# Kernel tuning notes

Hardware: AMD Instinct MI355X
Metric: run time of the kernel (lower is better)

Reference implementation:

```python
import jax, jax.numpy as jnp
import numpy as np

V, D, H, KVH, HD, I, L, T_MAX, THETA = 32000, 1024, 16, 4, 64, 2816, 2, 2048, 10000.0
EPS = 1e-5


def rmsnorm(x, w):
    return x * jax.lax.rsqrt(jnp.mean(x * x, axis=-1, keepdims=True) + EPS) * w


def rope_cos_sin(T):
    inv = 1.0 / (THETA ** (jnp.arange(0, HD, 2, dtype=jnp.float32) / HD))  # [HD/2]
    ang = jnp.arange(T, dtype=jnp.float32)[:, None] * inv[None, :]         # [T, HD/2]
    return jnp.cos(ang), jnp.sin(ang)


def apply_rope(x, cos, sin):
    # x: [B, T, h, HD]; interleaved complex pairs as in torch.view_as_complex
    x0 = x[..., 0::2]
    x1 = x[..., 1::2]
    c = cos[None, :, None, :]
    s = sin[None, :, None, :]
    o0 = x0 * c - x1 * s
    o1 = x0 * s + x1 * c
    return jnp.stack([o0, o1], axis=-1).reshape(x.shape)


def setup_inputs() -> dict:
    key = jax.random.key(0)
    ks = jax.random.split(key, 12)
    sc = 0.02
    return {
        "toks": jax.random.randint(ks[0], (1, 2048), 0, V),
        "embed": jax.random.normal(ks[1], (V, D), jnp.float32) * sc,
        "Wq": jax.random.normal(ks[2], (L, D, H * HD), jnp.float32) * sc,
        "Wk": jax.random.normal(ks[3], (L, D, KVH * HD), jnp.float32) * sc,
        "Wv": jax.random.normal(ks[4], (L, D, KVH * HD), jnp.float32) * sc,
        "Wo": jax.random.normal(ks[5], (L, H * HD, D), jnp.float32) * sc,
        "Wgate": jax.random.normal(ks[6], (L, D, I), jnp.float32) * sc,
        "Wup": jax.random.normal(ks[7], (L, D, I), jnp.float32) * sc,
        "Wdown": jax.random.normal(ks[8], (L, I, D), jnp.float32) * sc,
        "ln1_w": jnp.ones((L, D), jnp.float32),
        "ln2_w": jnp.ones((L, D), jnp.float32),
        "norm_w": jnp.ones((D,), jnp.float32),
        "Wlm": jax.random.normal(ks[9], (D, V), jnp.float32) * sc,
    }


def reference(toks, embed, Wq, Wk, Wv, Wo, Wgate, Wup, Wdown, ln1_w, ln2_w, norm_w, Wlm):
    B, T = toks.shape
    cos, sin = rope_cos_sin(T)
    causal = jnp.tril(jnp.ones((T, T), dtype=bool))
    add_mask = jnp.where(causal, 0.0, -jnp.inf).astype(jnp.float32)  # [T, T]
    n_rep = H // KVH
    scale = 1.0 / np.sqrt(HD)

    x = embed[toks]  # [B, T, D]
    for l in range(L):
        h = rmsnorm(x, ln1_w[l])
        q = (h @ Wq[l]).reshape(B, T, H, HD)
        k = (h @ Wk[l]).reshape(B, T, KVH, HD)
        v = (h @ Wv[l]).reshape(B, T, KVH, HD)
        q = apply_rope(q, cos, sin)
        k = apply_rope(k, cos, sin)
        k = jnp.repeat(k, n_rep, axis=2)  # GQA repeat_kv -> [B, T, H, HD]
        v = jnp.repeat(v, n_rep, axis=2)
        # materialized scores [B, H, T, T] (faithful to source)
        scores = jnp.einsum('bqhd,bkhd->bhqk', q, k) * scale + add_mask[None, None]
        probs = jax.nn.softmax(scores, axis=-1)
        attn = jnp.einsum('bhqk,bkhd->bqhd', probs, v).reshape(B, T, H * HD)
        x = x + attn @ Wo[l]
        h = rmsnorm(x, ln2_w[l])
        x = x + (jax.nn.silu(h @ Wgate[l]) * (h @ Wup[l])) @ Wdown[l]

    x = rmsnorm(x, norm_w)
    return x @ Wlm  # [B, T, V]
```

## Files before the change

kernel.cpp:

```cpp
#include <hip/hip_runtime.h>

#define T_SEQ 2048
#define DMODEL 1024
#define NH 16
#define NKV 4
#define HEAD_DIM 64
#define FFDIM 2816
#define NVOCAB 32000

#define QBLK 64
#define KBLK 128
#define KSS 72
#define VTS 136
#define PSS 136

using u16 = unsigned short;
typedef __bf16 bf16x8 __attribute__((ext_vector_type(8)));
typedef float f32x4 __attribute__((ext_vector_type(4)));

__device__ __forceinline__ float b2f(u16 u) {
    union { unsigned int i; float f; } v; v.i = ((unsigned int)u) << 16; return v.f;
}
__device__ __forceinline__ u16 f2b(float f) {
    unsigned int u = __builtin_bit_cast(unsigned int, f);
    unsigned int r = (u + 0x7FFFu + ((u >> 16) & 1u)) >> 16;
    return (u16)r;
}
__device__ __forceinline__ void gload16(const u16* g, u16* l) {
    __builtin_amdgcn_global_load_lds(
        (const __attribute__((address_space(1))) void*)g,
        (__attribute__((address_space(3))) void*)l, 16, 0, 0);
}

__global__ __launch_bounds__(256) void embed_kernel(const int* __restrict__ toks,
                                                    const float* __restrict__ emb,
                                                    float* __restrict__ x) {
    int idx = blockIdx.x * 256 + threadIdx.x;
    int t = idx >> 10, d = idx & 1023;
    x[idx] = emb[(size_t)toks[t] * DMODEL + d];
}

__global__ __launch_bounds__(256) void rmsnorm_kernel(const float* __restrict__ x,
                                                      const float* __restrict__ w,
                                                      u16* __restrict__ out) {
    __shared__ float red[256];
    const int row = blockIdx.x, tid = threadIdx.x;
    const float* xr = x + (size_t)row * DMODEL;
    float vals[4]; float ss = 0.f;
#pragma unroll
    for (int i = 0; i < 4; i++) { float v = xr[tid + 256 * i]; vals[i] = v; ss += v * v; }
    red[tid] = ss; __syncthreads();
    for (int s = 128; s > 0; s >>= 1) { if (tid < s) red[tid] += red[tid + s]; __syncthreads(); }
    float inv = rsqrtf(red[0] * (1.0f / DMODEL) + 1e-5f);
#pragma unroll
    for (int i = 0; i < 4; i++) {
        int c = tid + 256 * i;
        out[(size_t)row * DMODEL + c] = f2b(vals[i] * inv * w[c]);
    }
}

__global__ __launch_bounds__(256) void tcast_kernel(const float* __restrict__ in,
                                                    u16* __restrict__ out, int K, int N) {
    __shared__ float tile[32][33];
    int bx = blockIdx.x * 32;
    int by = blockIdx.y * 32;
    int tx = threadIdx.x & 31, ty = threadIdx.x >> 5;
#pragma unroll
    for (int i = 0; i < 32; i += 8)
        tile[ty + i][tx] = in[(size_t)(by + ty + i) * N + bx + tx];
    __syncthreads();
#pragma unroll
    for (int i = 0; i < 32; i += 8)
        out[(size_t)(bx + ty + i) * K + by + tx] = f2b(tile[tx][ty + i]);
}

__global__ __launch_bounds__(256) void vtcast_kernel(const float* __restrict__ fqkv,
                                                     u16* __restrict__ vt) {
    __shared__ float tile[32][33];
    int bx = blockIdx.x * 32;
    int by = blockIdx.y * 32;
    int tx = threadIdx.x & 31, ty = threadIdx.x >> 5;
#pragma unroll
    for (int i = 0; i < 32; i += 8)
        tile[ty + i][tx] = fqkv[(size_t)(by + ty + i) * 1536 + 1280 + bx + tx];
    __syncthreads();
#pragma unroll
    for (int i = 0; i < 32; i += 8)
        vt[(size_t)(bx + ty + i) * T_SEQ + by + tx] = f2b(tile[tx][ty + i]);
}

__global__ __launch_bounds__(256) void gemm_bt_kernel(const u16* __restrict__ A,
                                                      const u16* __restrict__ BT,
                                                      float* __restrict__ C,
                                                      int N, int K) {
    __shared__ __align__(16) u16 As[2][128 * 32];
    __shared__ __align__(16) u16 Bs[2][128 * 32];
    const int tid = threadIdx.x;
    const int gx = gridDim.x;
    const int nwg = gx * gridDim.y;
    const int hwid = blockIdx.y * gx + blockIdx.x;
    const int q = nwg >> 3, r = nwg & 7;
    const int xcd = hwid & 7, rem = hwid >> 3;
    const int wgid = (xcd < r ? xcd * (q + 1) : r * (q + 1) + (xcd - r) * q) + rem;
    const int brow = wgid % gx, bcol = wgid / gx;

    const int w = tid >> 6, lane = tid & 63;
    const int wr = w >> 1, wc = w & 1;
    const int lg = lane >> 4, lr = lane & 15;

    f32x4 acc[4][4] = {};

    const int srow = w * 32 + (lane >> 2);
    const int scol = (lane & 3) << 3;
    const u16* gA = A + (size_t)(brow * 128 + srow) * K + scol;
    const u16* gB = BT + (size_t)(bcol * 128 + srow) * K + scol;
    const int lofs0 = (w * 32) * 32;
    const int lofs1 = (w * 32 + 16) * 32;

    const int nt = K >> 5;
    gload16(gA, &As[0][lofs0]);
    gload16(gA + (size_t)16 * K, &As[0][lofs1]);
    gload16(gB, &Bs[0][lofs0]);
    gload16(gB + (size_t)16 * K, &Bs[0][lofs1]);
    __syncthreads();

    int cur = 0;
    for (int t = 0; t < nt; t++) {
        if (t + 1 < nt) {
            const int kb = (t + 1) << 5;
            gload16(gA + kb, &As[cur ^ 1][lofs0]);
            gload16(gA + (size_t)16 * K + kb, &As[cur ^ 1][lofs1]);
            gload16(gB + kb, &Bs[cur ^ 1][lofs0]);
            gload16(gB + (size_t)16 * K + kb, &Bs[cur ^ 1][lofs1]);
        }
        bf16x8 aF[4], bF[4];
#pragma unroll
        for (int m = 0; m < 4; m++)
            aF[m] = *(const bf16x8*)(&As[cur][(wr * 64 + m * 16 + lr) * 32 + lg * 8]);
#pragma unroll
        for (int n = 0; n < 4; n++)
            bF[n] = *(const bf16x8*)(&Bs[cur][(wc * 64 + n * 16 + lr) * 32 + lg * 8]);
#pragma unroll
        for (int m = 0; m < 4; m++)
#pragma unroll
            for (int n = 0; n < 4; n++)
                acc[m][n] = __builtin_amdgcn_mfma_f32_16x16x32_bf16(aF[m], bF[n], acc[m][n], 0, 0, 0);
        __syncthreads();
        cur ^= 1;
    }

#pragma unroll
    for (int m = 0; m < 4; m++)
#pragma unroll
        for (int n = 0; n < 4; n++)
#pragma unroll
            for (int j = 0; j < 4; j++) {
                int row = brow * 128 + wr * 64 + m * 16 + lg * 4 + j;
                int col = bcol * 128 + wc * 64 + n * 16 + lr;
                C[(size_t)row * N + col] = acc[m][n][j];
            }
}

__device__ __forceinline__ int bs_off(int c, int k) {
    return c * 40 + ((((k >> 3) ^ ((c >> 3) & 3)) << 3) | (k & 7));
}

__global__ __launch_bounds__(256) void gemm_f32b_kernel(const u16* __restrict__ A,
                                                        const float* __restrict__ B,
                                                        float* __restrict__ C,
                                                        int N, int K) {
    __shared__ __align__(16) u16 As[128 * 40];
    __shared__ __align__(16) u16 Bs[128 * 40];
    const int tid = threadIdx.x;
    const int brow = blockIdx.y, bcol = blockIdx.x;
    const int wid = tid >> 6, lane = tid & 63;
    const int wr = wid >> 1, wc = wid & 1;
    const int lg = lane >> 4, lr = lane & 15;

    f32x4 acc[4][4] = {};
    const int ar = tid >> 2, ac = (tid & 3) << 3;
    const int bk = tid >> 4, bc = (tid & 15) << 3;

    for (int kb = 0; kb < K; kb += 32) {
        {
            const u16* ga = A + (size_t)(brow * 128 + ar) * K + kb + ac;
            *(uint4*)(&As[ar * 40 + ac]) = *(const uint4*)ga;
            *(uint4*)(&As[(ar + 64) * 40 + ac]) = *(const uint4*)(ga + (size_t)64 * K);
        }
        {
            const float* gb = B + (size_t)(kb + bk) * N + bcol * 128 + bc;
            float4 a0 = *(const float4*)gb;
            float4 a1 = *(const float4*)(gb + 4);
            float4 b0 = *(const float4*)(gb + (size_t)16 * N);
            float4 b1 = *(const float4*)(gb + (size_t)16 * N + 4);
            float f0[8] = {a0.x, a0.y, a0.z, a0.w, a1.x, a1.y, a1.z, a1.w};
            float f1[8] = {b0.x, b0.y, b0.z, b0.w, b1.x, b1.y, b1.z, b1.w};
#pragma unroll
            for (int i = 0; i < 8; i++) {
                Bs[bs_off(bc + i, bk)] = f2b(f0[i]);
                Bs[bs_off(bc + i, bk + 16)] = f2b(f1[i]);
            }
        }
        __syncthreads();

        bf16x8 aF[4], bF[4];
#pragma unroll
        for (int m = 0; m < 4; m++)
            aF[m] = *(const bf16x8*)(&As[(wr * 64 + m * 16 + lr) * 40 + lg * 8]);
#pragma unroll
        for (int n = 0; n < 4; n++) {
            int c = wc * 64 + n * 16 + lr;
            bF[n] = *(const bf16x8*)(&Bs[c * 40 + ((lg ^ ((c >> 3) & 3)) << 3)]);
        }
#pragma unroll
        for (int m = 0; m < 4; m++)
#pragma unroll
            for (int n = 0; n < 4; n++)
                acc[m][n] = __builtin_amdgcn_mfma_f32_16x16x32_bf16(aF[m], bF[n], acc[m][n], 0, 0, 0);
        __syncthreads();
    }

#pragma unroll
    for (int m = 0; m < 4; m++)
#pragma unroll
        for (int n = 0; n < 4; n++)
#pragma unroll
            for (int j = 0; j < 4; j++) {
                int row = brow * 128 + wr * 64 + m * 16 + lg * 4 + j;
                int col = bcol * 128 + wc * 64 + n * 16 + lr;
                C[(size_t)row * N + col] = acc[m][n][j];
            }
}

__global__ __launch_bounds__(256) void rope_kernel(const float* __restrict__ in,
                                                   u16* __restrict__ out, int heads,
                                                   int instride, int incoloff) {
    int idx = blockIdx.x * 256 + threadIdx.x;
    int total = T_SEQ * heads * 32;
    if (idx >= total) return;
    int i = idx & 31;
    int rest = idx >> 5;
    int t = rest / heads, hh = rest - t * heads;
    float inv = expf(-(float)i * (9.210340371976184f / 32.0f));
    float ang = (float)t * inv;
    float c = cosf(ang), s = sinf(ang);
    size_t src = (size_t)t * instride + incoloff + hh * HEAD_DIM + 2 * i;
    size_t dst = (size_t)rest * HEAD_DIM + 2 * i;
    float x0 = in[src], x1 = in[src + 1];
    out[dst]     = f2b(x0 * c - x1 * s);
    out[dst + 1] = f2b(x0 * s + x1 * c);
}

__global__ __launch_bounds__(256) void fattn_kernel(const u16* __restrict__ q,
                                                    const u16* __restrict__ k,
                                                    const u16* __restrict__ vt,
                                                    u16* __restrict__ out) {
    __shared__ __align__(16) u16 Ks[KBLK * KSS];
    __shared__ __align__(16) u16 Vt[HEAD_DIM * VTS];
    __shared__ __align__(16) u16 Ps[QBLK * PSS];
    const int tid = threadIdx.x;
    const int qb0 = blockIdx.x * QBLK, h = blockIdx.y, kvh = h >> 2;
    const int w = tid >> 6, lane = tid & 63;
    const int lg = lane >> 4, lr = lane & 15;

    bf16x8 qf0, qf1;
    {
        const u16* src = q + ((size_t)(qb0 + w * 16 + lr) * NH + h) * HEAD_DIM;
        qf0 = *(const bf16x8*)(src + lg * 8);
        qf1 = *(const bf16x8*)(src + 32 + lg * 8);
    }

    f32x4 acc_o[4] = {};
    float m_run[4] = {-1e30f, -1e30f, -1e30f, -1e30f};
    float l_run[4] = {0.f, 0.f, 0.f, 0.f};

    const int ntiles = (qb0 + QBLK - 1) / KBLK + 1;

    for (int kt = 0; kt < ntiles; kt++) {
        const int kb = kt * KBLK;
        __syncthreads();
        for (int c = tid; c < KBLK * 8; c += 256) {
            int row = c >> 3, c8 = (c & 7) << 3;
            *(uint4*)(&Ks[row * KSS + c8]) =
                *(const uint4*)(k + ((size_t)(kb + row) * NKV + kvh) * HEAD_DIM + c8);
        }
        for (int c = tid; c < HEAD_DIM * 16; c += 256) {
            int d = c >> 4, c16 = (c & 15) << 3;
            *(uint4*)(&Vt[d * VTS + c16]) =
                *(const uint4*)(vt + (size_t)(kvh * HEAD_DIM + d) * T_SEQ + kb + c16);
        }
        __syncthreads();

        f32x4 s[8] = {};
#pragma unroll
        for (int n = 0; n < 8; n++) {
            bf16x8 kf0 = *(const bf16x8*)(&Ks[(n * 16 + lr) * KSS + lg * 8]);
            bf16x8 kf1 = *(const bf16x8*)(&Ks[(n * 16 + lr) * KSS + 32 + lg * 8]);
            s[n] = __builtin_amdgcn_mfma_f32_16x16x32_bf16(qf0, kf0, s[n], 0, 0, 0);
            s[n] = __builtin_amdgcn_mfma_f32_16x16x32_bf16(qf1, kf1, s[n], 0, 0, 0);
        }

#pragma unroll
        for (int j = 0; j < 4; j++) {
            int q_g = qb0 + w * 16 + lg * 4 + j;
            float sv[8];
            float tmax = -1e30f;
#pragma unroll
            for (int n = 0; n < 8; n++) {
                float xx = s[n][j] * 0.125f;
                if (kb + n * 16 + lr > q_g) xx = -1e30f;
                sv[n] = xx;
                tmax = fmaxf(tmax, xx);
            }
#pragma unroll
            for (int mm = 1; mm < 16; mm <<= 1) tmax = fmaxf(tmax, __shfl_xor(tmax, mm));
            float mn = fmaxf(m_run[j], tmax);
            float sc = __expf(m_run[j] - mn);
            m_run[j] = mn;
            float rsum = 0.f;
#pragma unroll
            for (int n = 0; n < 8; n++) {
                float p = __expf(sv[n] - mn);
                rsum += p;
                Ps[(w * 16 + lg * 4 + j) * PSS + n * 16 + lr] = f2b(p);
            }
#pragma unroll
            for (int mm = 1; mm < 16; mm <<= 1) rsum += __shfl_xor(rsum, mm);
            l_run[j] = l_run[j] * sc + rsum;
#pragma unroll
            for (int n = 0; n < 4; n++) acc_o[n][j] *= sc;
        }

#pragma unroll
        for (int ks = 0; ks < 4; ks++) {
            bf16x8 pf = *(const bf16x8*)(&Ps[(w * 16 + lr) * PSS + ks * 32 + lg * 8]);
#pragma unroll
            for (int n = 0; n < 4; n++) {
                bf16x8 vf = *(const bf16x8*)(&Vt[(n * 16 + lr) * VTS + ks * 32 + lg * 8]);
                acc_o[n] = __builtin_amdgcn_mfma_f32_16x16x32_bf16(pf, vf, acc_o[n], 0, 0, 0);
            }
        }
    }

#pragma unroll
    for (int n = 0; n < 4; n++)
#pragma unroll
        for (int j = 0; j < 4; j++) {
            int t = qb0 + w * 16 + lg * 4 + j;
            int d = n * 16 + lr;
            out[((size_t)t * NH + h) * HEAD_DIM + d] = f2b(acc_o[n][j] / l_run[j]);
        }
}

__global__ __launch_bounds__(256) void silu_mul_kernel(const float* __restrict__ gu,
                                                       u16* __restrict__ out) {
    int t = blockIdx.x;
    int c = blockIdx.y * 256 + threadIdx.x;
    float gv = gu[(size_t)t * 5632 + c];
    float uv = gu[(size_t)t * 5632 + 2816 + c];
    float s = gv / (1.f + __expf(-gv));
    out[(size_t)t * FFDIM + c] = f2b(s * uv);
}

__global__ __launch_bounds__(256) void add_kernel(float* __restrict__ x,
                                                  const float* __restrict__ y, int n) {
    int i = blockIdx.x * 256 + threadIdx.x;
    if (i < n) x[i] += y[i];
}

extern "C" void kernel_launch(void* const* d_in, const int* in_sizes, int n_in,
                              void* d_out, int out_size, void* d_ws, size_t ws_size,
                              hipStream_t stream) {
    const int*   toks = (const int*)d_in[0];
    const float* emb  = (const float*)d_in[1];
    const float* Wq   = (const float*)d_in[2];
    const float* Wk   = (const float*)d_in[3];
    const float* Wv   = (const float*)d_in[4];
    const float* Wo   = (const float*)d_in[5];
    const float* Wg   = (const float*)d_in[6];
    const float* Wu   = (const float*)d_in[7];
    const float* Wd   = (const float*)d_in[8];
    const float* ln1  = (const float*)d_in[9];
    const float* ln2  = (const float*)d_in[10];
    const float* nw   = (const float*)d_in[11];
    const float* Wlm  = (const float*)d_in[12];

    char* ob = (char*)d_out;
    const size_t MB = 1024 * 1024;
    float* x    = (float*)(ob + 0 * MB);
    float* fqkv = (float*)(ob + 8 * MB);
    float* fGU  = (float*)(ob + 20 * MB);
    float* fA   = (float*)(ob + 64 * MB);
    u16* vt     = (u16*)  (ob + 72 * MB);
    u16* qb     = (u16*)  (ob + 74 * MB);
    u16* kb     = (u16*)  (ob + 78 * MB);
    u16* attnb  = (u16*)  (ob + 80 * MB);
    u16* ffb    = (u16*)  (ob + 84 * MB);
    size_t woff = 96 * MB;
    auto walloc = [&](size_t elems) {
        u16* p = (u16*)(ob + woff);
        woff += ((elems * 2 + 255) & ~(size_t)255);
        return p;
    };
    u16 *WqkvT[2], *WoT[2], *WguT[2], *WdT[2];
    for (int l = 0; l < 2; l++) {
        WqkvT[l] = walloc((size_t)1536 * DMODEL);
        WoT[l]   = walloc((size_t)DMODEL * DMODEL);
        WguT[l]  = walloc((size_t)5632 * DMODEL);
        WdT[l]   = walloc((size_t)DMODEL * FFDIM);
    }
    u16* h = (u16*)d_ws;
    bool ws_big = ws_size >= 72 * MB;
    u16* WlmT = ws_big ? (u16*)((char*)d_ws + 4 * MB) : nullptr;
    (void)in_sizes; (void)n_in; (void)out_size;

    dim3 blk(256);
    auto tcast = [&](const float* in, u16* out, int K, int N) {
        tcast_kernel<<<dim3(N / 32, K / 32), blk, 0, stream>>>(in, out, K, N);
    };
    auto gemm_bt = [&](const u16* A, const u16* BT, float* C, int N, int K) {
        dim3 g(T_SEQ / 128, N / 128);
        gemm_bt_kernel<<<g, blk, 0, stream>>>(A, BT, C, N, K);
    };

    for (int l = 0; l < 2; l++) {
        tcast(Wq + (size_t)l * DMODEL * NH * HEAD_DIM,  WqkvT[l],                    DMODEL, NH * HEAD_DIM);
        tcast(Wk + (size_t)l * DMODEL * NKV * HEAD_DIM, WqkvT[l] + (size_t)1024 * DMODEL, DMODEL, NKV * HEAD_DIM);
        tcast(Wv + (size_t)l * DMODEL * NKV * HEAD_DIM, WqkvT[l] + (size_t)1280 * DMODEL, DMODEL, NKV * HEAD_DIM);
        tcast(Wo + (size_t)l * DMODEL * DMODEL,         WoT[l],  DMODEL, DMODEL);
        tcast(Wg + (size_t)l * DMODEL * FFDIM,          WguT[l],                     DMODEL, FFDIM);
        tcast(Wu + (size_t)l * DMODEL * FFDIM,          WguT[l] + (size_t)FFDIM * DMODEL, DMODEL, FFDIM);
        tcast(Wd + (size_t)l * FFDIM * DMODEL,          WdT[l],  FFDIM, DMODEL);
    }
    if (WlmT) tcast(Wlm, WlmT, DMODEL, NVOCAB);

    embed_kernel<<<dim3(T_SEQ * DMODEL / 256), blk, 0, stream>>>(toks, emb, x);

    for (int l = 0; l < 2; l++) {
        rmsnorm_kernel<<<dim3(T_SEQ), blk, 0, stream>>>(x, ln1 + (size_t)l * DMODEL, h);
        gemm_bt(h, WqkvT[l], fqkv, 1536, DMODEL);
        rope_kernel<<<dim3(T_SEQ * NH * 32 / 256), blk, 0, stream>>>(fqkv, qb, NH, 1536, 0);
        rope_kernel<<<dim3(T_SEQ * NKV * 32 / 256), blk, 0, stream>>>(fqkv, kb, NKV, 1536, 1024);
        vtcast_kernel<<<dim3(8, T_SEQ / 32), blk, 0, stream>>>(fqkv, vt);
        fattn_kernel<<<dim3(T_SEQ / QBLK, NH), blk, 0, stream>>>(qb, kb, vt, attnb);
        gemm_bt(attnb, WoT[l], fA, DMODEL, DMODEL);
        add_kernel<<<dim3(T_SEQ * DMODEL / 256), blk, 0, stream>>>(x, fA, T_SEQ * DMODEL);

        rmsnorm_kernel<<<dim3(T_SEQ), blk, 0, stream>>>(x, ln2 + (size_t)l * DMODEL, h);
        gemm_bt(h, WguT[l], fGU, 5632, DMODEL);
        silu_mul_kernel<<<dim3(T_SEQ, FFDIM / 256), blk, 0, stream>>>(fGU, ffb);
        gemm_bt(ffb, WdT[l], fA, DMODEL, FFDIM);
        add_kernel<<<dim3(T_SEQ * DMODEL / 256), blk, 0, stream>>>(x, fA, T_SEQ * DMODEL);
    }

    rmsnorm_kernel<<<dim3(T_SEQ), blk, 0, stream>>>(x, nw, h);
    if (WlmT) {
        gemm_bt(h, WlmT, (float*)d_out, NVOCAB, DMODEL);
    } else {
        dim3 g(NVOCAB / 128, T_SEQ / 128);
        gemm_f32b_kernel<<<g, blk, 0, stream>>>(h, Wlm, (float*)d_out, NVOCAB, DMODEL);
    }
}
```

Before: 851.1 us.

## Triple-buffer GEMM loads, emit bf16 intermediates, fuse residual add into GEMM epilogue

The GEMM kernel goes from a double-buffered to a triple-buffered LDS pipeline, with explicit vmcnt waits and raw barriers, so global loads for tile t+2 overlap compute on tile t. The QKV and gate/up projections now write bf16 instead of fp32, which halves the traffic into rope, vtcast and silu_mul. The Wo and Wdown GEMMs add directly into the residual x, removing the separate add kernels and the fA buffer. Rounding intermediates to bf16 slightly changes numerics, and the larger LDS footprint may reduce occupancy.

Result: slower. 887.9 us (+4.3%).

```diff
diff --git a/kernel.cpp b/kernel.cpp
--- a/kernel.cpp
+++ b/kernel.cpp
@@ -74,9 +74,9 @@
         out[(size_t)(bx + ty + i) * K + by + tx] = f2b(tile[tx][ty + i]);
 }
 
-__global__ __launch_bounds__(256) void vtcast_kernel(const float* __restrict__ fqkv,
+__global__ __launch_bounds__(256) void vtcast_kernel(const u16* __restrict__ fqkv,
                                                      u16* __restrict__ vt) {
-    __shared__ float tile[32][33];
+    __shared__ u16 tile[32][33];
     int bx = blockIdx.x * 32;
     int by = blockIdx.y * 32;
     int tx = threadIdx.x & 31, ty = threadIdx.x >> 5;
@@ -86,15 +86,16 @@
     __syncthreads();
 #pragma unroll
     for (int i = 0; i < 32; i += 8)
-        vt[(size_t)(bx + ty + i) * T_SEQ + by + tx] = f2b(tile[tx][ty + i]);
-}
-
+        vt[(size_t)(bx + ty + i) * T_SEQ + by + tx] = tile[tx][ty + i];
+}
+
+template<bool OUT_BF16, bool ADD>
 __global__ __launch_bounds__(256) void gemm_bt_kernel(const u16* __restrict__ A,
                                                       const u16* __restrict__ BT,
-                                                      float* __restrict__ C,
+                                                      void* __restrict__ Cp,
                                                       int N, int K) {
-    __shared__ __align__(16) u16 As[2][128 * 32];
-    __shared__ __align__(16) u16 Bs[2][128 * 32];
+    __shared__ __align__(16) u16 As[3][128 * 32];
+    __shared__ __align__(16) u16 Bs[3][128 * 32];
     const int tid = threadIdx.x;
     const int gx = gridDim.x;
     const int nwg = gx * gridDim.y;
@@ -114,24 +115,30 @@
     const int scol = (lane & 3) << 3;
     const u16* gA = A + (size_t)(brow * 128 + srow) * K + scol;
     const u16* gB = BT + (size_t)(bcol * 128 + srow) * K + scol;
+    const size_t koff16 = (size_t)16 * K;
     const int lofs0 = (w * 32) * 32;
     const int lofs1 = (w * 32 + 16) * 32;
 
     const int nt = K >> 5;
-    gload16(gA, &As[0][lofs0]);
-    gload16(gA + (size_t)16 * K, &As[0][lofs1]);
-    gload16(gB, &Bs[0][lofs0]);
-    gload16(gB + (size_t)16 * K, &Bs[0][lofs1]);
-    __syncthreads();
+    auto STAGE = [&](int t, int buf) {
+        const int kb = t << 5;
+        gload16(gA + kb, &As[buf][lofs0]);
+        gload16(gA + koff16 + kb, &As[buf][lofs1]);
+        gload16(gB + kb, &Bs[buf][lofs0]);
+        gload16(gB + koff16 + kb, &Bs[buf][lofs1]);
+    };
+
+    STAGE(0, 0);
+    STAGE(1, 1);
+    asm volatile("s_waitcnt vmcnt(4)" ::: "memory");
+    __builtin_amdgcn_s_barrier();
+    __builtin_amdgcn_sched_barrier(0);
 
     int cur = 0;
     for (int t = 0; t < nt; t++) {
-        if (t + 1 < nt) {
-            const int kb = (t + 1) << 5;
-            gload16(gA + kb, &As[cur ^ 1][lofs0]);
-            gload16(gA + (size_t)16 * K + kb, &As[cur ^ 1][lofs1]);
-            gload16(gB + kb, &Bs[cur ^ 1][lofs0]);
-            gload16(gB + (size_t)16 * K + kb, &Bs[cur ^ 1][lofs1]);
+        if (t + 2 < nt) {
+            int nb = cur + 2; if (nb >= 3) nb -= 3;
+            STAGE(t + 2, nb);
         }
         bf16x8 aF[4], bF[4];
 #pragma unroll
@@ -145,8 +152,11 @@
 #pragma unroll
             for (int n = 0; n < 4; n++)
                 acc[m][n] = __builtin_amdgcn_mfma_f32_16x16x32_bf16(aF[m], bF[n], acc[m][n], 0, 0, 0);
-        __syncthreads();
-        cur ^= 1;
+        if (t + 2 < nt) asm volatile("s_waitcnt vmcnt(4) lgkmcnt(0)" ::: "memory");
+        else            asm volatile("s_waitcnt vmcnt(0) lgkmcnt(0)" ::: "memory");
+        __builtin_amdgcn_s_barrier();
+        __builtin_amdgcn_sched_barrier(0);
+        cur = (cur == 2) ? 0 : cur + 1;
     }
 
 #pragma unroll
@@ -157,7 +167,15 @@
             for (int j = 0; j < 4; j++) {
                 int row = brow * 128 + wr * 64 + m * 16 + lg * 4 + j;
                 int col = bcol * 128 + wc * 64 + n * 16 + lr;
-                C[(size_t)row * N + col] = acc[m][n][j];
+                size_t idx = (size_t)row * N + col;
+                float v = acc[m][n][j];
+                if constexpr (OUT_BF16) {
+                    ((u16*)Cp)[idx] = f2b(v);
+                } else if constexpr (ADD) {
+                    ((float*)Cp)[idx] = ((const float*)Cp)[idx] + v;
+                } else {
+                    ((float*)Cp)[idx] = v;
+                }
             }
 }
 
@@ -232,7 +250,7 @@
             }
 }
 
-__global__ __launch_bounds__(256) void rope_kernel(const float* __restrict__ in,
+__global__ __launch_bounds__(256) void rope_kernel(const u16* __restrict__ in,
                                                    u16* __restrict__ out, int heads,
                                                    int instride, int incoloff) {
     int idx = blockIdx.x * 256 + threadIdx.x;
@@ -246,7 +264,7 @@
     float c = cosf(ang), s = sinf(ang);
     size_t src = (size_t)t * instride + incoloff + hh * HEAD_DIM + 2 * i;
     size_t dst = (size_t)rest * HEAD_DIM + 2 * i;
-    float x0 = in[src], x1 = in[src + 1];
+    float x0 = b2f(in[src]), x1 = b2f(in[src + 1]);
     out[dst]     = f2b(x0 * c - x1 * s);
     out[dst + 1] = f2b(x0 * s + x1 * c);
 }
@@ -352,20 +370,14 @@
         }
 }
 
-__global__ __launch_bounds__(256) void silu_mul_kernel(const float* __restrict__ gu,
+__global__ __launch_bounds__(256) void silu_mul_kernel(const u16* __restrict__ gu,
                                                        u16* __restrict__ out) {
     int t = blockIdx.x;
     int c = blockIdx.y * 256 + threadIdx.x;
-    float gv = gu[(size_t)t * 5632 + c];
-    float uv = gu[(size_t)t * 5632 + 2816 + c];
+    float gv = b2f(gu[(size_t)t * 5632 + c]);
+    float uv = b2f(gu[(size_t)t * 5632 + 2816 + c]);
     float s = gv / (1.f + __expf(-gv));
     out[(size_t)t * FFDIM + c] = f2b(s * uv);
-}
-
-__global__ __launch_bounds__(256) void add_kernel(float* __restrict__ x,
-                                                  const float* __restrict__ y, int n) {
-    int i = blockIdx.x * 256 + threadIdx.x;
-    if (i < n) x[i] += y[i];
 }
 
 extern "C" void kernel_launch(void* const* d_in, const int* in_sizes, int n_in,
@@ -388,15 +400,14 @@
     char* ob = (char*)d_out;
     const size_t MB = 1024 * 1024;
     float* x    = (float*)(ob + 0 * MB);
-    float* fqkv = (float*)(ob + 8 * MB);
-    float* fGU  = (float*)(ob + 20 * MB);
-    float* fA   = (float*)(ob + 64 * MB);
-    u16* vt     = (u16*)  (ob + 72 * MB);
-    u16* qb     = (u16*)  (ob + 74 * MB);
-    u16* kb     = (u16*)  (ob + 78 * MB);
-    u16* attnb  = (u16*)  (ob + 80 * MB);
-    u16* ffb    = (u16*)  (ob + 84 * MB);
-    size_t woff = 96 * MB;
+    u16* fqkv   = (u16*)  (ob + 8 * MB);
+    u16* fGU    = (u16*)  (ob + 16 * MB);
+    u16* vt     = (u16*)  (ob + 40 * MB);
+    u16* qb     = (u16*)  (ob + 42 * MB);
+    u16* kb     = (u16*)  (ob + 47 * MB);
+    u16* attnb  = (u16*)  (ob + 48 * MB);
+    u16* ffb    = (u16*)  (ob + 52 * MB);
+    size_t woff = 64 * MB;
     auto walloc = [&](size_t elems) {
         u16* p = (u16*)(ob + woff);
         woff += ((elems * 2 + 255) & ~(size_t)255);
@@ -418,17 +429,22 @@
     auto tcast = [&](const float* in, u16* out, int K, int N) {
         tcast_kernel<<<dim3(N / 32, K / 32), blk, 0, stream>>>(in, out, K, N);
     };
-    auto gemm_bt = [&](const u16* A, const u16* BT, float* C, int N, int K) {
+    auto gemm_f32 = [&](const u16* A, const u16* BT, float* C, int N, int K, bool add) {
         dim3 g(T_SEQ / 128, N / 128);
-        gemm_bt_kernel<<<g, blk, 0, stream>>>(A, BT, C, N, K);
+        if (add) gemm_bt_kernel<false, true><<<g, blk, 0, stream>>>(A, BT, (void*)C, N, K);
+        else     gemm_bt_kernel<false, false><<<g, blk, 0, stream>>>(A, BT, (void*)C, N, K);
     };
+    auto gemm_b16 = [&](const u16* A, const u16* BT, u16* C, int N, int K) {
+        dim3 g(T_SEQ / 128, N / 128);
+        gemm_bt_kernel<true, false><<<g, blk, 0, stream>>>(A, BT, (void*)C, N, K);
+    };
 
     for (int l = 0; l < 2; l++) {
-        tcast(Wq + (size_t)l * DMODEL * NH * HEAD_DIM,  WqkvT[l],                    DMODEL, NH * HEAD_DIM);
+        tcast(Wq + (size_t)l * DMODEL * NH * HEAD_DIM,  WqkvT[l],                         DMODEL, NH * HEAD_DIM);
         tcast(Wk + (size_t)l * DMODEL * NKV * HEAD_DIM, WqkvT[l] + (size_t)1024 * DMODEL, DMODEL, NKV * HEAD_DIM);
         tcast(Wv + (size_t)l * DMODEL * NKV * HEAD_DIM, WqkvT[l] + (size_t)1280 * DMODEL, DMODEL, NKV * HEAD_DIM);
         tcast(Wo + (size_t)l * DMODEL * DMODEL,         WoT[l],  DMODEL, DMODEL);
-        tcast(Wg + (size_t)l * DMODEL * FFDIM,          WguT[l],                     DMODEL, FFDIM);
+        tcast(Wg + (size_t)l * DMODEL * FFDIM,          WguT[l],                          DMODEL, FFDIM);
         tcast(Wu + (size_t)l * DMODEL * FFDIM,          WguT[l] + (size_t)FFDIM * DMODEL, DMODEL, FFDIM);
         tcast(Wd + (size_t)l * FFDIM * DMODEL,          WdT[l],  FFDIM, DMODEL);
     }
@@ -438,24 +454,22 @@
 
     for (int l = 0; l < 2; l++) {
         rmsnorm_kernel<<<dim3(T_SEQ), blk, 0, stream>>>(x, ln1 + (size_t)l * DMODEL, h);
-        gemm_bt(h, WqkvT[l], fqkv, 1536, DMODEL);
+        gemm_b16(h, WqkvT[l], fqkv, 1536, DMODEL);
         rope_kernel<<<dim3(T_SEQ * NH * 32 / 256), blk, 0, stream>>>(fqkv, qb, NH, 1536, 0);
         rope_kernel<<<dim3(T_SEQ * NKV * 32 / 256), blk, 0, stream>>>(fqkv, kb, NKV, 1536, 1024);
         vtcast_kernel<<<dim3(8, T_SEQ / 32), blk, 0, stream>>>(fqkv, vt);
         fattn_kernel<<<dim3(T_SEQ / QBLK, NH), blk, 0, stream>>>(qb, kb, vt, attnb);
-        gemm_bt(attnb, WoT[l], fA, DMODEL, DMODEL);
-        add_kernel<<<dim3(T_SEQ * DMODEL / 256), blk, 0, stream>>>(x, fA, T_SEQ * DMODEL);
+        gemm_f32(attnb, WoT[l], x, DMODEL, DMODEL, true);
 
         rmsnorm_kernel<<<dim3(T_SEQ), blk, 0, stream>>>(x, ln2 + (size_t)l * DMODEL, h);
-        gemm_bt(h, WguT[l], fGU, 5632, DMODEL);
+        gemm_b16(h, WguT[l], fGU, 5632, DMODEL);
         silu_mul_kernel<<<dim3(T_SEQ, FFDIM / 256), blk, 0, stream>>>(fGU, ffb);
-        gemm_bt(ffb, WdT[l], fA, DMODEL, FFDIM);
-        add_kernel<<<dim3(T_SEQ * DMODEL / 256), blk, 0, stream>>>(x, fA, T_SEQ * DMODEL);
+        gemm_f32(ffb, WdT[l], x, DMODEL, FFDIM, true);
     }
 
     rmsnorm_kernel<<<dim3(T_SEQ), blk, 0, stream>>>(x, nw, h);
     if (WlmT) {
-        gemm_bt(h, WlmT, (float*)d_out, NVOCAB, DMODEL);
+        gemm_f32(h, WlmT, (float*)d_out, NVOCAB, DMODEL, false);
     } else {
         dim3 g(NVOCAB / 128, T_SEQ / 128);
         gemm_f32b_kernel<<<g, blk, 0, stream>>>(h, Wlm, (float*)d_out, NVOCAB, DMODEL);
```
